# Kernel tuning notes

Hardware: AMD Instinct MI355X
Metric: run time of the kernel (lower is better)

The kernel has to match this reference:

```python
import jax, jax.numpy as jnp
from jax import lax
import numpy as np

BETA = 0.9   # snn.Leaky(beta=0.9)
THR = 1.0    # snntorch default threshold, reset_mechanism='subtract'

@jax.custom_vjp
def spike(x):
    return (x > 0.0).astype(x.dtype)

def _spike_fwd(x):
    return spike(x), x

def _spike_bwd(x, g):
    # snntorch surrogate.atan (alpha=2): dS/dx = 1 / (1 + (pi*x)^2)
    return (g / (1.0 + (jnp.pi * x) ** 2),)

spike.defvjp(_spike_fwd, _spike_bwd)

def lif(inp, mem):
    # snntorch Leaky: reset based on PREVIOUS mem, detached; subtract mechanism
    reset = lax.stop_gradient(spike(mem - THR))
    mem = BETA * mem + inp - reset * THR
    return spike(mem - THR), mem

def conv1d(x, w, b):
    # x: (B, Cin, L), w: (Cout, Cin, K), VALID padding
    y = lax.conv_general_dilated(x, w, window_strides=(1,), padding='VALID',
                                 dimension_numbers=('NCH', 'OIH', 'NCH'))
    return y + b[None, :, None]

def setup_inputs() -> dict:
    key = jax.random.key(0)
    ks = jax.random.split(key, 11)
    B, L, T, num_c = 1024, 30, 100, 10
    def init(k, shape, fan_in):
        bound = 1.0 / np.sqrt(fan_in)
        return jax.random.uniform(k, shape, jnp.float32, -bound, bound)
    return {
        'x':   jax.random.normal(ks[0], (B, 1, L, T), jnp.float32),
        'w1':  init(ks[1], (16, 1, 7), 1 * 7),   'b1': init(ks[2], (16,), 7),
        'w2':  init(ks[3], (32, 16, 5), 16 * 5), 'b2': init(ks[4], (32,), 80),
        'w3':  init(ks[5], (64, 32, 3), 32 * 3), 'b3': init(ks[6], (64,), 96),
        'fw1': init(ks[7], (256, 64 * 18), 64 * 18), 'fb1': init(ks[8], (256,), 64 * 18),
        'fw2': init(ks[9], (num_c, 256), 256),       'fb2': init(ks[10], (num_c,), 256),
    }

def reference(x, w1, b1, w2, b2, w3, b3, fw1, fb1, fw2, fb2):
    B = x.shape[0]
    num_c = fw2.shape[0]
    xt_seq = jnp.transpose(x, (3, 0, 1, 2))  # (T, B, 1, 30)
    mems = (jnp.zeros((B, 16, 24), x.dtype),  # after conv1 (k=7): 30->24
            jnp.zeros((B, 32, 20), x.dtype),  # after conv2 (k=5): 24->20
            jnp.zeros((B, 64, 18), x.dtype),  # after conv3 (k=3): 20->18
            jnp.zeros((B, 256), x.dtype),
            jnp.zeros((B, num_c), x.dtype))
    def step(mems, xt):
        m1, m2, m3, m4, m5 = mems
        h = conv1d(xt, w1, b1); s, m1 = lif(h, m1)
        h = conv1d(s, w2, b2);  s, m2 = lif(h, m2)
        h = conv1d(s, w3, b3);  s, m3 = lif(h, m3)
        h = s.reshape(B, -1) @ fw1.T + fb1; s, m4 = lif(h, m4)
        h = s @ fw2.T + fb2;               s, m5 = lif(h, m5)
        return (m1, m2, m3, m4, m5), s
    _, spk_rec = lax.scan(step, mems, xt_seq)
    return spk_rec  # (T, B, num_c) -- matches torch.stack(spk_rec)
```

## Files before the change

kernel.cpp:

```cpp
#include <hip/hip_runtime.h>
#include <stdint.h>

#define BETA 0.9f

__global__ void transpose_fw1(const float* __restrict__ A, float* __restrict__ At) {
    __shared__ float tile[32][33];
    const int i0 = blockIdx.x * 32;
    const int j0 = blockIdx.y * 32;
    const int tx = threadIdx.x, ty = threadIdx.y;
    for (int r = ty; r < 32; r += 8)
        tile[r][tx] = A[(j0 + r) * 1152 + i0 + tx];
    __syncthreads();
    for (int r = ty; r < 32; r += 8)
        At[(i0 + r) * 256 + j0 + tx] = tile[tx][r];
}

__global__ __launch_bounds__(512, 4) void snn_main(
    const float* __restrict__ x,
    const float* __restrict__ w1, const float* __restrict__ b1,
    const float* __restrict__ w2, const float* __restrict__ b2,
    const float* __restrict__ w3, const float* __restrict__ b3,
    const float* __restrict__ fw1T,
    const float* __restrict__ fb1,
    const float* __restrict__ fw2, const float* __restrict__ fb2,
    float* __restrict__ out)
{
    const int b    = blockIdx.x;
    const int tid  = threadIdx.x;
    const int e    = tid >> 8;
    const int tl   = tid & 255;
    const int lane = tid & 63;
    const int ew   = (tid >> 6) & 3;

    __shared__ float w2L[16 * 5 * 32];
    __shared__ float w3L[32 * 3 * 64];
    __shared__ float pacc[2][4][256];
    __shared__ float s1e[2][16 * 24 + 4];
    __shared__ float s4[2][256];
    __shared__ unsigned long long masks[2][18];
    __shared__ unsigned int rm1[2][2][16];
    __shared__ unsigned int cm2[2][2][20];

    const int c1 = tl & 15;
    const int l1 = tl >> 4;
    const int c2 = tl & 31;
    const int lg2 = tl >> 5;
    const int l02 = (lg2 < 4) ? 3 * lg2 : 12 + 2 * (lg2 - 4);
    const int nl2 = (lg2 < 4) ? 3 : 2;
    const int c3 = lane;
    const int l03 = ew * 5;
    const int nl3 = (ew < 3) ? 5 : 3;

    const unsigned wmask2 = (ew == 0) ? 0x3FFu :
                            (ew == 1) ? 0xFFC0u :
                            (ew == 2) ? 0xFF000u :
                                        0xFF0000u;

    for (int i = tid; i < 16 * 5 * 32; i += 512) {
        const int cc = i & 31, r = i >> 5;
        w2L[i] = w2[cc * 80 + r];
    }
    for (int i = tid; i < 32 * 3 * 64; i += 512) {
        const int cc = i & 63, r = i >> 6;
        w3L[i] = w3[cc * 96 + r];
    }
    if (tl < 16) { rm1[e][0][tl] = 0u; rm1[e][1][tl] = 0u; }
    if (tl < 20) { cm2[e][0][tl] = 0u; cm2[e][1][tl] = 0u; }
    if (tl < 4)  s1e[e][384 + tl] = 0.0f;

    float w1r[7];
#pragma unroll
    for (int k = 0; k < 7; ++k) w1r[k] = w1[c1 * 7 + k];
    const float b1r = b1[c1];
    const float b2r = b2[c2];
    const float b3r = b3[c3];
    const float fb1r = fb1[tl];
    const int jf = tl >> 4, chf = tl & 15;
    const float fb2r = (tl < 160 && chf == 0) ? fb2[jf] : 0.0f;
    float fw2r[16];
    if (tl < 160) {
#pragma unroll
        for (int i = 0; i < 16; ++i) fw2r[i] = fw2[jf * 256 + i * 16 + chf];
    }

    float m1a = 0.f, m1b = 0.f;
    float m2[3] = {0.f, 0.f, 0.f};
    float m3[5] = {0.f, 0.f, 0.f, 0.f, 0.f};
    float m4 = 0.f, m5 = 0.f;

    const float* xb = x + (2 * b + e) * 3000;
    const int out_b = (2 * b + e) * 10;
    const float4* fw1Tv = reinterpret_cast<const float4*>(fw1T);

    float xr[7], xr2[7];
#pragma unroll
    for (int k = 0; k < 7; ++k) xr[k] = xb[(l1 + k) * 100];
#pragma unroll
    for (int k = 0; k < 7; ++k) xr2[k] = (tl < 128) ? xb[(16 + l1 + k) * 100] : 0.0f;

    __syncthreads();

    for (int t = 0; t < 100; ++t) {
        const int pb = t & 1, pn = pb ^ 1;

        {
            unsigned bits = 0u;
            float h = b1r;
#pragma unroll
            for (int k = 0; k < 7; ++k) h += xr[k] * w1r[k];
            float rs = (m1a > 1.0f) ? 1.0f : 0.0f;
            m1a = BETA * m1a + h - rs;
            float sa = (m1a > 1.0f) ? 1.0f : 0.0f;
            s1e[e][c1 * 24 + l1] = sa;
            if (sa != 0.0f) bits |= 1u << l1;
            if (tl < 128) {
                float h2 = b1r;
#pragma unroll
                for (int k = 0; k < 7; ++k) h2 += xr2[k] * w1r[k];
                float r2 = (m1b > 1.0f) ? 1.0f : 0.0f;
                m1b = BETA * m1b + h2 - r2;
                float sb = (m1b > 1.0f) ? 1.0f : 0.0f;
                s1e[e][c1 * 24 + 16 + l1] = sb;
                if (sb != 0.0f) bits |= 1u << (16 + l1);
            }
            if (bits) atomicOr(&rm1[e][pb][c1], bits);
        }
        {
            const int tt = (t < 99) ? t + 1 : 99;
#pragma unroll
            for (int k = 0; k < 7; ++k) xr[k] = xb[(l1 + k) * 100 + tt];
            if (tl < 128) {
#pragma unroll
                for (int k = 0; k < 7; ++k) xr2[k] = xb[(16 + l1 + k) * 100 + tt];
            }
        }
        __syncthreads();

        {
            if (tl < 16) rm1[e][pn][tl] = 0u;
            if (tl < 20) cm2[e][pn][tl] = 0u;
            float h[3] = {b2r, b2r, b2r};
#pragma unroll
            for (int ci = 0; ci < 16; ++ci) {
                const unsigned rmv =
                    __builtin_amdgcn_readfirstlane(rm1[e][pb][ci]);
                if ((rmv & wmask2) == 0u) continue;
                float win[7];
#pragma unroll
                for (int r = 0; r < 7; ++r) win[r] = s1e[e][ci * 24 + l02 + r];
                float wk[5];
#pragma unroll
                for (int k = 0; k < 5; ++k) wk[k] = w2L[(ci * 5 + k) * 32 + c2];
#pragma unroll
                for (int li = 0; li < 3; ++li)
                    if (li < nl2)
#pragma unroll
                        for (int k = 0; k < 5; ++k) h[li] += win[li + k] * wk[k];
            }
#pragma unroll
            for (int li = 0; li < 3; ++li)
                if (li < nl2) {
                    float rs = (m2[li] > 1.0f) ? 1.0f : 0.0f;
                    m2[li] = BETA * m2[li] + h[li] - rs;
                    if (m2[li] > 1.0f) atomicOr(&cm2[e][pb][l02 + li], 1u << c2);
                }
        }
        __syncthreads();

        {
            float h[5] = {b3r, b3r, b3r, b3r, b3r};
            const int wcnt = nl3 + 2;
#pragma unroll
            for (int wl = 0; wl < 7; ++wl) {
                if (wl >= wcnt) break;
                unsigned cm = __builtin_amdgcn_readfirstlane(cm2[e][pb][l03 + wl]);
                while (cm) {
                    const int ci = (int)__builtin_ctz(cm); cm &= cm - 1;
                    const float* wp = &w3L[ci * 192 + c3];
#pragma unroll
                    for (int k = 0; k < 3; ++k) {
                        const int li = wl - k;
                        if (li >= 0 && li < 5)
                            if (li < nl3)
                                h[li] += wp[k * 64];
                    }
                }
            }
#pragma unroll
            for (int li = 0; li < 5; ++li)
                if (li < nl3) {
                    float rs = (m3[li] > 1.0f) ? 1.0f : 0.0f;
                    m3[li] = BETA * m3[li] + h[li] - rs;
                    float s = (m3[li] > 1.0f) ? 1.0f : 0.0f;
                    unsigned long long mk = __ballot(s != 0.0f);
                    if (lane == 0) masks[e][l03 + li] = mk;
                }
        }
        __syncthreads();

        {
            float4 acc4; acc4.x = acc4.y = acc4.z = acc4.w = 0.0f;
#pragma unroll 1
            for (int l = ew; l < 18; l += 4) {
                const unsigned* mp = (const unsigned*)&masks[e][l];
                const unsigned mlo = __builtin_amdgcn_readfirstlane(mp[0]);
                const unsigned mhi = __builtin_amdgcn_readfirstlane(mp[1]);
                unsigned long long mk = ((unsigned long long)mhi << 32) | mlo;
                while (mk) {
                    float4 f0, f1, f2, f3;
                    f0.x=f0.y=f0.z=f0.w=0.f; f1=f0; f2=f0; f3=f0;
                    int c;
                    c = (int)__builtin_ctzll(mk); mk &= mk - 1;
                    f0 = fw1Tv[(c * 18 + l) * 64 + lane];
                    if (mk) { c = (int)__builtin_ctzll(mk); mk &= mk - 1;
                              f1 = fw1Tv[(c * 18 + l) * 64 + lane]; }
                    if (mk) { c = (int)__builtin_ctzll(mk); mk &= mk - 1;
                              f2 = fw1Tv[(c * 18 + l) * 64 + lane]; }
                    if (mk) { c = (int)__builtin_ctzll(mk); mk &= mk - 1;
                              f3 = fw1Tv[(c * 18 + l) * 64 + lane]; }
                    acc4.x += f0.x; acc4.y += f0.y; acc4.z += f0.z; acc4.w += f0.w;
                    acc4.x += f1.x; acc4.y += f1.y; acc4.z += f1.z; acc4.w += f1.w;
                    acc4.x += f2.x; acc4.y += f2.y; acc4.z += f2.z; acc4.w += f2.w;
                    acc4.x += f3.x; acc4.y += f3.y; acc4.z += f3.z; acc4.w += f3.w;
                }
            }
            ((float4*)&pacc[e][ew][0])[lane] = acc4;
        }
        __syncthreads();

        {
            float acc = fb1r + pacc[e][0][tl] + pacc[e][1][tl]
                             + pacc[e][2][tl] + pacc[e][3][tl];
            float rs = (m4 > 1.0f) ? 1.0f : 0.0f;
            m4 = BETA * m4 + acc - rs;
            s4[e][tl] = (m4 > 1.0f) ? 1.0f : 0.0f;
        }
        __syncthreads();

        if (tl < 160) {
            float p = 0.f;
#pragma unroll
            for (int i = 0; i < 16; ++i)
                p += s4[e][i * 16 + chf] * fw2r[i];
            p += __shfl_xor(p, 8, 16);
            p += __shfl_xor(p, 4, 16);
            p += __shfl_xor(p, 2, 16);
            p += __shfl_xor(p, 1, 16);
            if (chf == 0) {
                float h = fb2r + p;
                float rs = (m5 > 1.0f) ? 1.0f : 0.0f;
                m5 = BETA * m5 + h - rs;
                out[t * 10240 + out_b + jf] = (m5 > 1.0f) ? 1.0f : 0.0f;
            }
        }
    }
}

extern "C" void kernel_launch(void* const* d_in, const int* in_sizes, int n_in,
                              void* d_out, int out_size, void* d_ws, size_t ws_size,
                              hipStream_t stream) {
    const float* x   = (const float*)d_in[0];
    const float* w1  = (const float*)d_in[1];
    const float* b1  = (const float*)d_in[2];
    const float* w2  = (const float*)d_in[3];
    const float* b2  = (const float*)d_in[4];
    const float* w3  = (const float*)d_in[5];
    const float* b3  = (const float*)d_in[6];
    const float* fw1 = (const float*)d_in[7];
    const float* fb1 = (const float*)d_in[8];
    const float* fw2 = (const float*)d_in[9];
    const float* fb2 = (const float*)d_in[10];
    float* out  = (float*)d_out;
    float* fw1T = (float*)d_ws;

    dim3 tb(32, 8);
    dim3 tg(1152 / 32, 256 / 32);
    transpose_fw1<<<tg, tb, 0, stream>>>(fw1, fw1T);
    snn_main<<<512, 512, 0, stream>>>(x, w1, b1, w2, b2, w3, b3,
                                      fw1T, fb1, fw2, fb2, out);
}
```

Before: 741.4 us.

## Double threads per sample to 512 and split per-thread work across more threads

Block size goes from 512 to 1024 threads, so each of the two samples in a block gets 512 threads instead of 256. Conv1, conv2, conv3 and the fc1 sparse gather now give each thread fewer output positions, and fc1 partial sums come from 8 waves instead of 4. The fc2 weights are read from global memory each step instead of being held in registers, to lower register pressure. The goal is more parallelism within each serial timestep loop, at the cost of a tighter register budget, more idle threads in some stages, and more partial-sum reduction work.

```diff
diff --git a/kernel.cpp b/kernel.cpp
--- a/kernel.cpp
+++ b/kernel.cpp
@@ -15,7 +15,7 @@
         At[(i0 + r) * 256 + j0 + tx] = tile[tx][r];
 }
 
-__global__ __launch_bounds__(512, 4) void snn_main(
+__global__ __launch_bounds__(1024, 8) void snn_main(
     const float* __restrict__ x,
     const float* __restrict__ w1, const float* __restrict__ b1,
     const float* __restrict__ w2, const float* __restrict__ b2,
@@ -27,15 +27,15 @@
 {
     const int b    = blockIdx.x;
     const int tid  = threadIdx.x;
-    const int e    = tid >> 8;
-    const int tl   = tid & 255;
+    const int e    = tid >> 9;
+    const int tl   = tid & 511;
     const int lane = tid & 63;
-    const int ew   = (tid >> 6) & 3;
+    const int ew   = tl >> 6;
 
     __shared__ float w2L[16 * 5 * 32];
     __shared__ float w3L[32 * 3 * 64];
-    __shared__ float pacc[2][4][256];
-    __shared__ float s1e[2][16 * 24 + 4];
+    __shared__ float pacc[2][8][256];
+    __shared__ float s1e[2][16 * 24];
     __shared__ float s4[2][256];
     __shared__ unsigned long long masks[2][18];
     __shared__ unsigned int rm1[2][2][16];
@@ -44,29 +44,32 @@
     const int c1 = tl & 15;
     const int l1 = tl >> 4;
     const int c2 = tl & 31;
-    const int lg2 = tl >> 5;
-    const int l02 = (lg2 < 4) ? 3 * lg2 : 12 + 2 * (lg2 - 4);
-    const int nl2 = (lg2 < 4) ? 3 : 2;
+    const int g2 = tl >> 5;
+    const int l02 = (g2 < 12) ? g2 : 12 + 2 * (g2 - 12);
+    const int nl2 = (g2 < 12) ? 1 : 2;
     const int c3 = lane;
-    const int l03 = ew * 5;
-    const int nl3 = (ew < 3) ? 5 : 3;
-
-    const unsigned wmask2 = (ew == 0) ? 0x3FFu :
-                            (ew == 1) ? 0xFFC0u :
-                            (ew == 2) ? 0xFF000u :
+    const int l03 = (ew < 2) ? 3 * ew : 6 + 2 * (ew - 2);
+    const int nl3 = (ew < 2) ? 3 : 2;
+
+    const unsigned wmask2 = (ew == 0) ? 0x3Fu :
+                            (ew == 1) ? 0xFCu :
+                            (ew == 2) ? 0x3F0u :
+                            (ew == 3) ? 0xFC0u :
+                            (ew == 4) ? 0x3F00u :
+                            (ew == 5) ? 0xFC00u :
+                            (ew == 6) ? 0xFF000u :
                                         0xFF0000u;
 
-    for (int i = tid; i < 16 * 5 * 32; i += 512) {
+    for (int i = tid; i < 16 * 5 * 32; i += 1024) {
         const int cc = i & 31, r = i >> 5;
         w2L[i] = w2[cc * 80 + r];
     }
-    for (int i = tid; i < 32 * 3 * 64; i += 512) {
+    for (int i = tid; i < 32 * 3 * 64; i += 1024) {
         const int cc = i & 63, r = i >> 6;
         w3L[i] = w3[cc * 96 + r];
     }
     if (tl < 16) { rm1[e][0][tl] = 0u; rm1[e][1][tl] = 0u; }
     if (tl < 20) { cm2[e][0][tl] = 0u; cm2[e][1][tl] = 0u; }
-    if (tl < 4)  s1e[e][384 + tl] = 0.0f;
 
     float w1r[7];
 #pragma unroll
@@ -74,91 +77,66 @@
     const float b1r = b1[c1];
     const float b2r = b2[c2];
     const float b3r = b3[c3];
-    const float fb1r = fb1[tl];
+    const float fb1r = (tl < 256) ? fb1[tl] : 0.0f;
     const int jf = tl >> 4, chf = tl & 15;
     const float fb2r = (tl < 160 && chf == 0) ? fb2[jf] : 0.0f;
-    float fw2r[16];
-    if (tl < 160) {
-#pragma unroll
-        for (int i = 0; i < 16; ++i) fw2r[i] = fw2[jf * 256 + i * 16 + chf];
-    }
-
-    float m1a = 0.f, m1b = 0.f;
-    float m2[3] = {0.f, 0.f, 0.f};
-    float m3[5] = {0.f, 0.f, 0.f, 0.f, 0.f};
+
+    float m1 = 0.f;
+    float m2[2] = {0.f, 0.f};
+    float m3[3] = {0.f, 0.f, 0.f};
     float m4 = 0.f, m5 = 0.f;
 
     const float* xb = x + (2 * b + e) * 3000;
     const int out_b = (2 * b + e) * 10;
     const float4* fw1Tv = reinterpret_cast<const float4*>(fw1T);
 
-    float xr[7], xr2[7];
-#pragma unroll
-    for (int k = 0; k < 7; ++k) xr[k] = xb[(l1 + k) * 100];
-#pragma unroll
-    for (int k = 0; k < 7; ++k) xr2[k] = (tl < 128) ? xb[(16 + l1 + k) * 100] : 0.0f;
+    float xr[7];
+#pragma unroll
+    for (int k = 0; k < 7; ++k) xr[k] = (tl < 384) ? xb[(l1 + k) * 100] : 0.0f;
 
     __syncthreads();
 
     for (int t = 0; t < 100; ++t) {
         const int pb = t & 1, pn = pb ^ 1;
 
-        {
-            unsigned bits = 0u;
+        if (tl < 384) {
             float h = b1r;
 #pragma unroll
             for (int k = 0; k < 7; ++k) h += xr[k] * w1r[k];
-            float rs = (m1a > 1.0f) ? 1.0f : 0.0f;
-            m1a = BETA * m1a + h - rs;
-            float sa = (m1a > 1.0f) ? 1.0f : 0.0f;
+            float rs = (m1 > 1.0f) ? 1.0f : 0.0f;
+            m1 = BETA * m1 + h - rs;
+            float sa = (m1 > 1.0f) ? 1.0f : 0.0f;
             s1e[e][c1 * 24 + l1] = sa;
-            if (sa != 0.0f) bits |= 1u << l1;
-            if (tl < 128) {
-                float h2 = b1r;
-#pragma unroll
-                for (int k = 0; k < 7; ++k) h2 += xr2[k] * w1r[k];
-                float r2 = (m1b > 1.0f) ? 1.0f : 0.0f;
-                m1b = BETA * m1b + h2 - r2;
-                float sb = (m1b > 1.0f) ? 1.0f : 0.0f;
-                s1e[e][c1 * 24 + 16 + l1] = sb;
-                if (sb != 0.0f) bits |= 1u << (16 + l1);
-            }
-            if (bits) atomicOr(&rm1[e][pb][c1], bits);
-        }
-        {
+            if (sa != 0.0f) atomicOr(&rm1[e][pb][c1], 1u << l1);
             const int tt = (t < 99) ? t + 1 : 99;
 #pragma unroll
             for (int k = 0; k < 7; ++k) xr[k] = xb[(l1 + k) * 100 + tt];
-            if (tl < 128) {
-#pragma unroll
-                for (int k = 0; k < 7; ++k) xr2[k] = xb[(16 + l1 + k) * 100 + tt];
-            }
         }
         __syncthreads();
 
         {
             if (tl < 16) rm1[e][pn][tl] = 0u;
             if (tl < 20) cm2[e][pn][tl] = 0u;
-            float h[3] = {b2r, b2r, b2r};
+            float h[2] = {b2r, b2r};
 #pragma unroll
             for (int ci = 0; ci < 16; ++ci) {
                 const unsigned rmv =
                     __builtin_amdgcn_readfirstlane(rm1[e][pb][ci]);
                 if ((rmv & wmask2) == 0u) continue;
-                float win[7];
-#pragma unroll
-                for (int r = 0; r < 7; ++r) win[r] = s1e[e][ci * 24 + l02 + r];
+                float win[6];
+#pragma unroll
+                for (int r = 0; r < 6; ++r) win[r] = s1e[e][ci * 24 + l02 + r];
                 float wk[5];
 #pragma unroll
                 for (int k = 0; k < 5; ++k) wk[k] = w2L[(ci * 5 + k) * 32 + c2];
 #pragma unroll
-                for (int li = 0; li < 3; ++li)
+                for (int li = 0; li < 2; ++li)
                     if (li < nl2)
 #pragma unroll
                         for (int k = 0; k < 5; ++k) h[li] += win[li + k] * wk[k];
             }
 #pragma unroll
-            for (int li = 0; li < 3; ++li)
+            for (int li = 0; li < 2; ++li)
                 if (li < nl2) {
                     float rs = (m2[li] > 1.0f) ? 1.0f : 0.0f;
                     m2[li] = BETA * m2[li] + h[li] - rs;
@@ -168,10 +146,10 @@
         __syncthreads();
 
         {
-            float h[5] = {b3r, b3r, b3r, b3r, b3r};
+            float h[3] = {b3r, b3r, b3r};
             const int wcnt = nl3 + 2;
 #pragma unroll
-            for (int wl = 0; wl < 7; ++wl) {
+            for (int wl = 0; wl < 5; ++wl) {
                 if (wl >= wcnt) break;
                 unsigned cm = __builtin_amdgcn_readfirstlane(cm2[e][pb][l03 + wl]);
                 while (cm) {
@@ -180,14 +158,14 @@
 #pragma unroll
                     for (int k = 0; k < 3; ++k) {
                         const int li = wl - k;
-                        if (li >= 0 && li < 5)
+                        if (li >= 0 && li < 3)
                             if (li < nl3)
                                 h[li] += wp[k * 64];
                     }
                 }
             }
 #pragma unroll
-            for (int li = 0; li < 5; ++li)
+            for (int li = 0; li < 3; ++li)
                 if (li < nl3) {
                     float rs = (m3[li] > 1.0f) ? 1.0f : 0.0f;
                     m3[li] = BETA * m3[li] + h[li] - rs;
@@ -201,7 +179,7 @@
         {
             float4 acc4; acc4.x = acc4.y = acc4.z = acc4.w = 0.0f;
 #pragma unroll 1
-            for (int l = ew; l < 18; l += 4) {
+            for (int l = ew; l < 18; l += 8) {
                 const unsigned* mp = (const unsigned*)&masks[e][l];
                 const unsigned mlo = __builtin_amdgcn_readfirstlane(mp[0]);
                 const unsigned mhi = __builtin_amdgcn_readfirstlane(mp[1]);
@@ -228,9 +206,10 @@
         }
         __syncthreads();
 
-        {
-            float acc = fb1r + pacc[e][0][tl] + pacc[e][1][tl]
-                             + pacc[e][2][tl] + pacc[e][3][tl];
+        if (tl < 256) {
+            float acc = fb1r;
+#pragma unroll
+            for (int w = 0; w < 8; ++w) acc += pacc[e][w][tl];
             float rs = (m4 > 1.0f) ? 1.0f : 0.0f;
             m4 = BETA * m4 + acc - rs;
             s4[e][tl] = (m4 > 1.0f) ? 1.0f : 0.0f;
@@ -238,10 +217,11 @@
         __syncthreads();
 
         if (tl < 160) {
+            const float* wrow = fw2 + jf * 256;
             float p = 0.f;
 #pragma unroll
             for (int i = 0; i < 16; ++i)
-                p += s4[e][i * 16 + chf] * fw2r[i];
+                p += s4[e][i * 16 + chf] * wrow[i * 16 + chf];
             p += __shfl_xor(p, 8, 16);
             p += __shfl_xor(p, 4, 16);
             p += __shfl_xor(p, 2, 16);
@@ -276,6 +256,6 @@
     dim3 tb(32, 8);
     dim3 tg(1152 / 32, 256 / 32);
     transpose_fw1<<<tg, tb, 0, stream>>>(fw1, fw1T);
-    snn_main<<<512, 512, 0, stream>>>(x, w1, b1, w2, b2, w3, b3,
-                                      fw1T, fb1, fw2, fb2, out);
+    snn_main<<<512, 1024, 0, stream>>>(x, w1, b1, w2, b2, w3, b3,
+                                       fw1T, fb1, fw2, fb2, out);
 }
```

After: 1.131 ms. 1.53x slower.
